# Optimization experiments

Hardware: AMD Instinct MI355X
Metric: run time of the kernel (lower is better)

## Reference

```python
import jax, jax.numpy as jnp
import numpy as np

VOC, OUT, HID, CUR = 50257, 512, 64, 16
B, S = 32, 4096
EPS = 1e-5


def _ln(x, g, b):
    m = jnp.mean(x, axis=-1, keepdims=True)
    v = jnp.mean((x - m) ** 2, axis=-1, keepdims=True)
    return (x - m) * jax.lax.rsqrt(v + EPS) * g + b


def setup_inputs() -> dict:
    key = jax.random.key(0)
    ks = jax.random.split(key, 12)
    sd = 0.02
    return {
        "x": jax.random.randint(ks[0], (B, S), 0, VOC, dtype=jnp.int64),
        "emb": jax.random.normal(ks[1], (VOC, CUR), jnp.float32) * sd,
        "Wq": jax.random.normal(ks[2], (CUR, CUR), jnp.float32) * sd,
        "bq": jnp.zeros((CUR,), jnp.float32),
        "Wk": jax.random.normal(ks[3], (CUR, CUR), jnp.float32) * sd,
        "bk": jnp.zeros((CUR,), jnp.float32),
        "Wv": jax.random.normal(ks[4], (CUR, CUR), jnp.float32) * sd,
        "bv": jnp.zeros((CUR,), jnp.float32),
        "g_lim": jnp.ones((CUR,), jnp.float32),
        "b_lim": jnp.zeros((CUR,), jnp.float32),
        "Ws": jax.random.normal(ks[5], (HID + CUR, HID), jnp.float32) * sd,
        "bs": jnp.zeros((HID,), jnp.float32),
        "g_doubt": jnp.ones((HID,), jnp.float32),
        "b_doubt": jnp.zeros((HID,), jnp.float32),
        "Wd": jax.random.normal(ks[6], (HID + CUR, OUT), jnp.float32) * sd,
        "bd": jnp.zeros((OUT,), jnp.float32),
        "g_check": jnp.ones((OUT,), jnp.float32),
        "b_check": jnp.zeros((OUT,), jnp.float32),
    }


def reference(x, emb, Wq, bq, Wk, bk, Wv, bv, g_lim, b_lim, Ws, bs,
              g_doubt, b_doubt, Wd, bd, g_check, b_check):
    Bsz, Slen = x.shape
    n_chunks = Slen // CUR
    # [n_chunks, B, CUR] token ids per chunk
    xc = x.reshape(Bsz, n_chunks, CUR).transpose(1, 0, 2)
    sus0 = jnp.zeros((Bsz, CUR, HID), emb.dtype)
    scale = 1.0 / np.sqrt(CUR)

    def step(sus, ids):
        read = emb[ids]                                  # [B, CUR, CUR]
        q = read @ Wq + bq
        k = read @ Wk + bk
        v = read @ Wv + bv
        scores = jnp.einsum('bqd,bkd->bqk', q, k) * scale
        watch = jnp.einsum('bqk,bkd->bqd', jax.nn.softmax(scores, axis=-1), v)
        watch = _ln(watch, g_lim, b_lim)                 # dropout = identity (eval)
        combined = jnp.concatenate([watch, sus], axis=-1)  # [B, CUR, HID+CUR]
        sus_new = _ln(jax.nn.gelu(combined @ Ws + bs, approximate=False),
                      g_doubt, b_doubt)
        out = _ln(combined @ Wd + bd, g_check, b_check)  # [B, CUR, OUT]
        return sus_new, out

    _, outs = jax.lax.scan(step, sus0, xc)               # [n_chunks, B, CUR, OUT]
    return outs.transpose(1, 0, 2, 3).reshape(Bsz, Slen, OUT)
```

## Files before the change

kernel.cpp:

```cpp
#include <hip/hip_runtime.h>
#include <math.h>

#define VOCN 50257
#define OUTD 512
#define HIDD 64
#define CURD 16
#define BB   32
#define SS   4096
#define NCH  256
#define KDIM 80
#define LNEPS 1e-5f

#define WS_WHI   41943040
#define WS_WLO   (WS_WHI + 96*512*2)
#define WS_FLAGS (WS_WLO + 96*512*2)
#define NRECB    128
#define NOUTB    512
#define NTASKS   4096
#define NSLABS   16

#define DPP_ADD(x, ctrl) \
    ((x) + __int_as_float(__builtin_amdgcn_update_dpp( \
        0, __float_as_int(x), (ctrl), 0xf, 0xf, true)))

__device__ __forceinline__ float row16_sum(float x) {
    x = DPP_ADD(x, 0xB1);
    x = DPP_ADD(x, 0x4E);
    x = DPP_ADD(x, 0x141);
    x = DPP_ADD(x, 0x140);
    return x;
}

__device__ __forceinline__ float wave64_sum(float x) {
    float r = row16_sum(x);
    float a = __int_as_float(__builtin_amdgcn_readlane(__float_as_int(r), 0));
    float b = __int_as_float(__builtin_amdgcn_readlane(__float_as_int(r), 16));
    float c = __int_as_float(__builtin_amdgcn_readlane(__float_as_int(r), 32));
    float d = __int_as_float(__builtin_amdgcn_readlane(__float_as_int(r), 48));
    return (a + b) + (c + d);
}

__device__ __forceinline__ unsigned short f2bf(float x) {
    unsigned u = __float_as_uint(x);
    u += 0x7fffu + ((u >> 16) & 1u);
    return (unsigned short)(u >> 16);
}
__device__ __forceinline__ float bf2f(unsigned short h) {
    return __uint_as_float(((unsigned)h) << 16);
}

typedef __attribute__((ext_vector_type(8))) short bf16x8;
typedef __attribute__((ext_vector_type(4))) float f32x4;

__global__ __launch_bounds__(256) void attn_kernel(
    const int* __restrict__ x, const float* __restrict__ emb,
    const float* __restrict__ Wq, const float* __restrict__ bq,
    const float* __restrict__ Wk, const float* __restrict__ bk,
    const float* __restrict__ Wv, const float* __restrict__ bv,
    const float* __restrict__ g_lim, const float* __restrict__ b_lim,
    float* __restrict__ combined,
    const float* __restrict__ Wd,
    unsigned short* __restrict__ whi, unsigned short* __restrict__ wlo,
    unsigned int* __restrict__ flags)
{
    if (blockIdx.x == 0) {
        flags[threadIdx.x] = 0u;
        flags[threadIdx.x + 256] = 0u;
    }

    const int wid  = threadIdx.x >> 6;
    const int lane = threadIdx.x & 63;
    const int tile = blockIdx.x * 4 + wid;
    const int t = tile >> 5, b = tile & 31;
    const int i  = lane >> 2;
    const int jg = lane & 3;
    const int j0 = jg * 4;

    __shared__ __align__(16) float ldsT[4][4][16][20];
    float (*R)[20] = ldsT[wid][0];
    float (*Q)[20] = ldsT[wid][1];
    float (*K)[20] = ldsT[wid][2];
    float (*V)[20] = ldsT[wid][3];

    int myid = 0;
    if (lane < 16) myid = x[b * SS + t * CURD + lane];
    const int id_i = __shfl(myid, i, 64);

    float4 r4 = *(const float4*)(emb + (size_t)id_i * CURD + j0);
    *(float4*)&R[i][j0] = r4;

    float rrow[16];
    {
        float4 t0 = *(const float4*)&R[i][0];
        float4 t1 = *(const float4*)&R[i][4];
        float4 t2 = *(const float4*)&R[i][8];
        float4 t3 = *(const float4*)&R[i][12];
        rrow[0]=t0.x; rrow[1]=t0.y; rrow[2]=t0.z;  rrow[3]=t0.w;
        rrow[4]=t1.x; rrow[5]=t1.y; rrow[6]=t1.z;  rrow[7]=t1.w;
        rrow[8]=t2.x; rrow[9]=t2.y; rrow[10]=t2.z; rrow[11]=t2.w;
        rrow[12]=t3.x; rrow[13]=t3.y; rrow[14]=t3.z; rrow[15]=t3.w;
    }

    float4 q4 = *(const float4*)(bq + j0);
    float4 k4 = *(const float4*)(bk + j0);
    float4 v4 = *(const float4*)(bv + j0);
    #pragma unroll
    for (int k = 0; k < 16; ++k) {
        float rv = rrow[k];
        float4 wq4 = *(const float4*)(Wq + k * CURD + j0);
        float4 wk4 = *(const float4*)(Wk + k * CURD + j0);
        float4 wv4 = *(const float4*)(Wv + k * CURD + j0);
        q4.x = fmaf(rv, wq4.x, q4.x); q4.y = fmaf(rv, wq4.y, q4.y);
        q4.z = fmaf(rv, wq4.z, q4.z); q4.w = fmaf(rv, wq4.w, q4.w);
        k4.x = fmaf(rv, wk4.x, k4.x); k4.y = fmaf(rv, wk4.y, k4.y);
        k4.z = fmaf(rv, wk4.z, k4.z); k4.w = fmaf(rv, wk4.w, k4.w);
        v4.x = fmaf(rv, wv4.x, v4.x); v4.y = fmaf(rv, wv4.y, v4.y);
        v4.z = fmaf(rv, wv4.z, v4.z); v4.w = fmaf(rv, wv4.w, v4.w);
    }
    *(float4*)&Q[i][j0] = q4;
    *(float4*)&K[i][j0] = k4;
    *(float4*)&V[i][j0] = v4;

    float qrow[16];
    {
        float4 t0 = *(const float4*)&Q[i][0];
        float4 t1 = *(const float4*)&Q[i][4];
        float4 t2 = *(const float4*)&Q[i][8];
        float4 t3 = *(const float4*)&Q[i][12];
        qrow[0]=t0.x; qrow[1]=t0.y; qrow[2]=t0.z;  qrow[3]=t0.w;
        qrow[4]=t1.x; qrow[5]=t1.y; qrow[6]=t1.z;  qrow[7]=t1.w;
        qrow[8]=t2.x; qrow[9]=t2.y; qrow[10]=t2.z; qrow[11]=t2.w;
        qrow[12]=t3.x; qrow[13]=t3.y; qrow[14]=t3.z; qrow[15]=t3.w;
    }
    float sc[4];
    #pragma unroll
    for (int jj = 0; jj < 4; ++jj) {
        const int row = j0 + jj;
        float4 c0 = *(const float4*)&K[row][0];
        float4 c1 = *(const float4*)&K[row][4];
        float4 c2 = *(const float4*)&K[row][8];
        float4 c3 = *(const float4*)&K[row][12];
        float d0 = qrow[0]*c0.x + qrow[1]*c0.y + qrow[2]*c0.z + qrow[3]*c0.w;
        float d1 = qrow[4]*c1.x + qrow[5]*c1.y + qrow[6]*c1.z + qrow[7]*c1.w;
        float d2 = qrow[8]*c2.x + qrow[9]*c2.y + qrow[10]*c2.z + qrow[11]*c2.w;
        float d3 = qrow[12]*c3.x + qrow[13]*c3.y + qrow[14]*c3.z + qrow[15]*c3.w;
        sc[jj] = ((d0 + d1) + (d2 + d3)) * 0.25f;
    }

    float mx = fmaxf(fmaxf(sc[0], sc[1]), fmaxf(sc[2], sc[3]));
    mx = fmaxf(mx, __shfl_xor(mx, 1));
    mx = fmaxf(mx, __shfl_xor(mx, 2));
    float e0 = expf(sc[0]-mx), e1 = expf(sc[1]-mx),
          e2 = expf(sc[2]-mx), e3 = expf(sc[3]-mx);
    float es = (e0 + e1) + (e2 + e3);
    es += __shfl_xor(es, 1);
    es += __shfl_xor(es, 2);
    float rs = 1.f / es;
    float4 p4 = make_float4(e0*rs, e1*rs, e2*rs, e3*rs);
    *(float4*)&R[i][j0] = p4;

    float prow[16];
    {
        float4 t0 = *(const float4*)&R[i][0];
        float4 t1 = *(const float4*)&R[i][4];
        float4 t2 = *(const float4*)&R[i][8];
        float4 t3 = *(const float4*)&R[i][12];
        prow[0]=t0.x; prow[1]=t0.y; prow[2]=t0.z;  prow[3]=t0.w;
        prow[4]=t1.x; prow[5]=t1.y; prow[6]=t1.z;  prow[7]=t1.w;
        prow[8]=t2.x; prow[9]=t2.y; prow[10]=t2.z; prow[11]=t2.w;
        prow[12]=t3.x; prow[13]=t3.y; prow[14]=t3.z; prow[15]=t3.w;
    }
    float4 w4 = make_float4(0.f, 0.f, 0.f, 0.f);
    #pragma unroll
    for (int k = 0; k < 16; ++k) {
        float4 vk = *(const float4*)&V[k][j0];
        float pv = prow[k];
        w4.x = fmaf(pv, vk.x, w4.x); w4.y = fmaf(pv, vk.y, w4.y);
        w4.z = fmaf(pv, vk.z, w4.z); w4.w = fmaf(pv, vk.w, w4.w);
    }

    float s1 = (w4.x + w4.y) + (w4.z + w4.w);
    float s2 = (w4.x*w4.x + w4.y*w4.y) + (w4.z*w4.z + w4.w*w4.w);
    s1 += __shfl_xor(s1, 1); s1 += __shfl_xor(s1, 2);
    s2 += __shfl_xor(s2, 1); s2 += __shfl_xor(s2, 2);
    float m   = s1 * (1.f / 16.f);
    float var = s2 * (1.f / 16.f) - m * m;
    float inv = rsqrtf(var + LNEPS);
    float4 gl = *(const float4*)(g_lim + j0);
    float4 bl = *(const float4*)(b_lim + j0);
    float4 o;
    o.x = (w4.x - m) * inv * gl.x + bl.x;
    o.y = (w4.y - m) * inv * gl.y + bl.y;
    o.z = (w4.z - m) * inv * gl.z + bl.z;
    o.w = (w4.w - m) * inv * gl.w + bl.w;
    *(float4*)(combined + ((size_t)tile * CURD + i) * KDIM + j0) = o;

    if (blockIdx.x < 192) {
        int idx = blockIdx.x * 256 + threadIdx.x;
        int k = idx / 512, c = idx % 512;
        float v = (k < KDIM) ? Wd[(size_t)k * OUTD + c] : 0.f;
        unsigned short h = f2bf(v);
        unsigned short l = f2bf(v - bf2f(h));
        int s = k >> 5, kk = k & 31, g = kk >> 3, e = kk & 7;
        size_t o2 = (((size_t)(s * 512 + c)) * 4 + g) * 8 + e;
        whi[o2] = h;
        wlo[o2] = l;
    }
}

__global__ __launch_bounds__(256, 1) void fused_kernel(
    const float* __restrict__ Ws, const float* __restrict__ bs,
    const float* __restrict__ g_doubt, const float* __restrict__ b_doubt,
    float* __restrict__ combined,
    const unsigned short* __restrict__ Bhi,
    const unsigned short* __restrict__ Blo,
    const float* __restrict__ bd, const float* __restrict__ g_check,
    const float* __restrict__ b_check, float* __restrict__ out,
    unsigned int* __restrict__ flags)
{
    __shared__ __align__(16) unsigned short Ahi[32][104];
    __shared__ __align__(16) unsigned short Alo[32][104];
    __shared__ float red[4][32][2];
    __shared__ float s_G[4][64];
    __shared__ int s_tk;

    const int tid = threadIdx.x;
    if (tid == 0)
        s_tk = (int)__hip_atomic_fetch_add(&flags[0], 1u,
                    __ATOMIC_RELAXED, __HIP_MEMORY_SCOPE_AGENT);
    __syncthreads();
    const int role_tk = s_tk;

    if (role_tk < NRECB) {
        __builtin_amdgcn_s_setprio(1);
        const int wid = tid >> 6;
        const int c   = tid & 63;
        const int chain = role_tk * 4 + wid;
        const int b = chain >> 4;
        const int r = chain & 15;

        float Wsw[16];
        #pragma unroll
        for (int j = 0; j < 16; ++j) Wsw[j] = Ws[j * HIDD + c];

        float Wsp[64];
        float u = 0.f, w0 = 0.f;
        #pragma unroll
        for (int j = 0; j < 64; ++j) {
            float w   = Ws[(16 + j) * HIDD + c];
            float gdj = g_doubt[j];
            float bdj = b_doubt[j];
            Wsp[j] = gdj * w;
            u += Wsp[j];
            w0 = fmaf(bdj, w, w0);
        }
        const float bsc  = bs[c];
        const float gd_c = g_doubt[c];
        const float bd_c = b_doubt[c];

        size_t rowoff = ((size_t)b * CURD + r) * KDIM;
        const size_t stride = (size_t)BB * CURD * KDIM;

        float4 wc0, wc1, wc2, wc3;
        float4 wn0, wn1, wn2, wn3;
        {
            const float4* p0 = (const float4*)(combined + rowoff);
            wc0 = p0[0]; wc1 = p0[1]; wc2 = p0[2]; wc3 = p0[3];
            const float4* p1 = (const float4*)(combined + rowoff + stride);
            wn0 = p1[0]; wn1 = p1[1]; wn2 = p1[2]; wn3 = p1[3];
        }

        float P = 0.f, mp = 0.f, ip = 0.f, w0f = 0.f;
        float sv_store = 0.f;

        for (int t = 0; t < NCH; ++t) {
            __hip_atomic_store(&combined[rowoff + 16 + c], sv_store,
                               __ATOMIC_RELAXED, __HIP_MEMORY_SCOPE_AGENT);

            if ((t & 15) == 15) {
                asm volatile("s_waitcnt vmcnt(0)" ::: "memory");
                if (c == 0)
                    __hip_atomic_fetch_add(&flags[16 + (t >> 4) * 16], 1u,
                        __ATOMIC_RELAXED, __HIP_MEMORY_SCOPE_AGENT);
            }

            float4 wp0, wp1, wp2, wp3;
            if (t + 2 < NCH) {
                const float4* p2 = (const float4*)(combined + rowoff + 2 * stride);
                wp0 = p2[0]; wp1 = p2[1]; wp2 = p2[2]; wp3 = p2[3];
            } else {
                wp0 = wp1 = wp2 = wp3 = make_float4(0.f, 0.f, 0.f, 0.f);
            }

            float h0 = fmaf(ip, P - mp * u, bsc + w0f);
            float h1 = 0.f, h2 = 0.f, h3 = 0.f;
            h0 = fmaf(wc0.x, Wsw[0],  h0); h1 = fmaf(wc0.y, Wsw[1],  h1);
            h2 = fmaf(wc0.z, Wsw[2],  h2); h3 = fmaf(wc0.w, Wsw[3],  h3);
            h0 = fmaf(wc1.x, Wsw[4],  h0); h1 = fmaf(wc1.y, Wsw[5],  h1);
            h2 = fmaf(wc1.z, Wsw[6],  h2); h3 = fmaf(wc1.w, Wsw[7],  h3);
            h0 = fmaf(wc2.x, Wsw[8],  h0); h1 = fmaf(wc2.y, Wsw[9],  h1);
            h2 = fmaf(wc2.z, Wsw[10], h2); h3 = fmaf(wc2.w, Wsw[11], h3);
            h0 = fmaf(wc3.x, Wsw[12], h0); h1 = fmaf(wc3.y, Wsw[13], h1);
            h2 = fmaf(wc3.z, Wsw[14], h2); h3 = fmaf(wc3.w, Wsw[15], h3);
            float h = (h0 + h1) + (h2 + h3);

            float G = 0.5f * h * (1.f + erff(h * 0.70710678118654752f));

            s_G[wid][c] = G;
            const float4* gp = (const float4*)s_G[wid];

            float s1 = wave64_sum(G);
            float s2 = wave64_sum(G * G);
            float m   = s1 * (1.f / 64.f);
            float var = s2 * (1.f / 64.f) - m * m;
            float inv = rsqrtf(var + LNEPS);

            float p0=0.f,p1=0.f,p2=0.f,p3=0.f,p4=0.f,p5=0.f,p6=0.f,p7=0.f;
            #pragma unroll
            for (int bq = 0; bq < 4; ++bq) {
                float4 x0 = gp[bq*4+0], x1 = gp[bq*4+1];
                float4 x2 = gp[bq*4+2], x3 = gp[bq*4+3];
                p0 = fmaf(x0.x, Wsp[16*bq+0],  p0);
                p1 = fmaf(x0.y, Wsp[16*bq+1],  p1);
                p2 = fmaf(x0.z, Wsp[16*bq+2],  p2);
                p3 = fmaf(x0.w, Wsp[16*bq+3],  p3);
                p4 = fmaf(x1.x, Wsp[16*bq+4],  p4);
                p5 = fmaf(x1.y, Wsp[16*bq+5],  p5);
                p6 = fmaf(x1.z, Wsp[16*bq+6],  p6);
                p7 = fmaf(x1.w, Wsp[16*bq+7],  p7);
                p0 = fmaf(x2.x, Wsp[16*bq+8],  p0);
                p1 = fmaf(x2.y, Wsp[16*bq+9],  p1);
                p2 = fmaf(x2.z, Wsp[16*bq+10], p2);
                p3 = fmaf(x2.w, Wsp[16*bq+11], p3);
                p4 = fmaf(x3.x, Wsp[16*bq+12], p4);
                p5 = fmaf(x3.y, Wsp[16*bq+13], p5);
                p6 = fmaf(x3.z, Wsp[16*bq+14], p6);
                p7 = fmaf(x3.w, Wsp[16*bq+15], p7);
            }
            P = ((p0 + p1) + (p2 + p3)) + ((p4 + p5) + (p6 + p7));

            sv_store = fmaf((G - m) * inv, gd_c, bd_c);
            mp = m; ip = inv; w0f = w0;
            wc0 = wn0; wc1 = wn1; wc2 = wn2; wc3 = wn3;
            wn0 = wp0; wn1 = wp1; wn2 = wp2; wn3 = wp3;
            rowoff += stride;
        }
        return;
    }

    const int lane  = tid & 63;
    const int wid   = tid >> 6;
    const int arowb = lane & 15;
    const int kg    = lane >> 4;

    int cols[8]; float bdv[8], gcv[8], bcv[8];
    #pragma unroll
    for (int n = 0; n < 8; ++n) {
        cols[n] = wid * 128 + n * 16 + arowb;
        bdv[n] = bd[cols[n]];
        gcv[n] = g_check[cols[n]];
        bcv[n] = b_check[cols[n]];
    }

    for (;;) {
        if (tid == 0)
            s_tk = (int)__hip_atomic_fetch_add(&flags[1], 1u,
                        __ATOMIC_RELAXED, __HIP_MEMORY_SCOPE_AGENT);
        __syncthreads();
        const int task = s_tk;
        if (task >= NTASKS) break;

        const int slab = task >> 8;
        if (tid == 0) {
            unsigned guard = 0;
            while (__hip_atomic_load(&flags[16 + slab * 16], __ATOMIC_RELAXED,
                                     __HIP_MEMORY_SCOPE_AGENT) < 512u
                   && guard < (1u << 20)) {
                __builtin_amdgcn_s_sleep(32);
                ++guard;
            }
        }
        __syncthreads();
        asm volatile("" ::: "memory");

        const size_t rowbase = (size_t)task * 32;

        {
            const float4* src4 = (const float4*)(combined + rowbase * KDIM);
            #pragma unroll
            for (int u2 = 0; u2 < 3; ++u2) {
                int idx = tid + 256 * u2;
                if (idx < 32 * 20) {
                    float4 v = src4[idx];
                    int rr = idx / 20, k4 = idx % 20;
                    float vs[4] = {v.x, v.y, v.z, v.w};
                    #pragma unroll
                    for (int e = 0; e < 4; ++e) {
                        unsigned short h = f2bf(vs[e]);
                        Ahi[rr][k4 * 4 + e] = h;
                        Alo[rr][k4 * 4 + e] = f2bf(vs[e] - bf2f(h));
                    }
                }
            }
            #pragma unroll
            for (int u2 = 0; u2 < 2; ++u2) {
                int idx = tid + 256 * u2;
                int rr = idx >> 4, kk = 80 + (idx & 15);
                Ahi[rr][kk] = 0;
                Alo[rr][kk] = 0;
            }
        }
        __syncthreads();

        bf16x8 a_hi[2][3], a_lo[2][3];
        #pragma unroll
        for (int ms = 0; ms < 2; ++ms)
            #pragma unroll
            for (int s = 0; s < 3; ++s) {
                a_hi[ms][s] = *(const bf16x8*)&Ahi[ms * 16 + arowb][s * 32 + kg * 8];
                a_lo[ms][s] = *(const bf16x8*)&Alo[ms * 16 + arowb][s * 32 + kg * 8];
            }

        f32x4 acc[2][8];
        #pragma unroll
        for (int ms = 0; ms < 2; ++ms)
            #pragma unroll
            for (int n = 0; n < 8; ++n) acc[ms][n] = (f32x4){0.f, 0.f, 0.f, 0.f};

        #pragma unroll
        for (int n = 0; n < 8; ++n) {
            #pragma unroll
            for (int s = 0; s < 3; ++s) {
                size_t off = (((size_t)(s * 512 + cols[n])) * 4 + kg) * 8;
                bf16x8 bh = *(const bf16x8*)(Bhi + off);
                bf16x8 bl = *(const bf16x8*)(Blo + off);
                acc[0][n] = __builtin_amdgcn_mfma_f32_16x16x32_bf16(a_hi[0][s], bh, acc[0][n], 0, 0, 0);
                acc[1][n] = __builtin_amdgcn_mfma_f32_16x16x32_bf16(a_hi[1][s], bh, acc[1][n], 0, 0, 0);
                acc[0][n] = __builtin_amdgcn_mfma_f32_16x16x32_bf16(a_lo[0][s], bh, acc[0][n], 0, 0, 0);
                acc[1][n] = __builtin_amdgcn_mfma_f32_16x16x32_bf16(a_lo[1][s], bh, acc[1][n], 0, 0, 0);
                acc[0][n] = __builtin_amdgcn_mfma_f32_16x16x32_bf16(a_hi[0][s], bl, acc[0][n], 0, 0, 0);
                acc[1][n] = __builtin_amdgcn_mfma_f32_16x16x32_bf16(a_hi[1][s], bl, acc[1][n], 0, 0, 0);
            }
        }

        #pragma unroll
        for (int ms = 0; ms < 2; ++ms) {
            float s1[4] = {0.f, 0.f, 0.f, 0.f};
            float s2[4] = {0.f, 0.f, 0.f, 0.f};
            #pragma unroll
            for (int n = 0; n < 8; ++n) {
                #pragma unroll
                for (int j = 0; j < 4; ++j) {
                    float v = acc[ms][n][j] + bdv[n];
                    acc[ms][n][j] = v;
                    s1[j] += v;
                    s2[j] = fmaf(v, v, s2[j]);
                }
            }
            #pragma unroll
            for (int j = 0; j < 4; ++j) {
                s1[j] = row16_sum(s1[j]);
                s2[j] = row16_sum(s2[j]);
            }
            if (arowb == 0) {
                #pragma unroll
                for (int j = 0; j < 4; ++j) {
                    red[wid][ms * 16 + kg * 4 + j][0] = s1[j];
                    red[wid][ms * 16 + kg * 4 + j][1] = s2[j];
                }
            }
        }
        __syncthreads();

        #pragma unroll
        for (int ms = 0; ms < 2; ++ms) {
            #pragma unroll
            for (int j = 0; j < 4; ++j) {
                const int rowl = ms * 16 + kg * 4 + j;
                float t1 = (red[0][rowl][0] + red[1][rowl][0])
                         + (red[2][rowl][0] + red[3][rowl][0]);
                float t2 = (red[0][rowl][1] + red[1][rowl][1])
                         + (red[2][rowl][1] + red[3][rowl][1]);
                float mm  = t1 * (1.f / 512.f);
                float var = t2 * (1.f / 512.f) - mm * mm;
                float iv  = rsqrtf(var + LNEPS);

                size_t R = rowbase + (size_t)rowl;
                int ii  = (int)(R & 15);
                int bb2 = (int)((R >> 4) & 31);
                int tt  = (int)(R >> 9);
                size_t orow = ((size_t)bb2 * SS + (size_t)tt * CURD + ii) * OUTD;

                #pragma unroll
                for (int n = 0; n < 8; ++n) {
                    out[orow + cols[n]] =
                        (acc[ms][n][j] - mm) * iv * gcv[n] + bcv[n];
                }
            }
        }
        __syncthreads();
    }
}

extern "C" void kernel_launch(void* const* d_in, const int* in_sizes, int n_in,
                              void* d_out, int out_size, void* d_ws, size_t ws_size,
                              hipStream_t stream)
{
    const int*   x       = (const int*)  d_in[0];
    const float* emb     = (const float*)d_in[1];
    const float* Wq      = (const float*)d_in[2];
    const float* bq      = (const float*)d_in[3];
    const float* Wk      = (const float*)d_in[4];
    const float* bk      = (const float*)d_in[5];
    const float* Wv      = (const float*)d_in[6];
    const float* bv      = (const float*)d_in[7];
    const float* g_lim   = (const float*)d_in[8];
    const float* b_lim   = (const float*)d_in[9];
    const float* Ws      = (const float*)d_in[10];
    const float* bs      = (const float*)d_in[11];
    const float* g_doubt = (const float*)d_in[12];
    const float* b_doubt = (const float*)d_in[13];
    const float* Wd      = (const float*)d_in[14];
    const float* bd      = (const float*)d_in[15];
    const float* g_check = (const float*)d_in[16];
    const float* b_check = (const float*)d_in[17];

    float* out      = (float*)d_out;
    float* combined = (float*)d_ws;
    unsigned short* whi = (unsigned short*)((char*)d_ws + WS_WHI);
    unsigned short* wlo = (unsigned short*)((char*)d_ws + WS_WLO);
    unsigned int*  flags = (unsigned int*)((char*)d_ws + WS_FLAGS);

    attn_kernel<<<dim3(NCH * BB / 4), dim3(256), 0, stream>>>(
        x, emb, Wq, bq, Wk, bk, Wv, bv, g_lim, b_lim, combined,
        Wd, whi, wlo, flags);

    fused_kernel<<<dim3(NRECB + NOUTB), dim3(256), 0, stream>>>(
        Ws, bs, g_doubt, b_doubt, combined, whi, wlo,
        bd, g_check, b_check, out, flags);
}
```

Baseline: 579.3 us.

## Preload each recurrence chain's watch rows into LDS and halve waves per block

```diff
diff --git a/kernel.cpp b/kernel.cpp
--- a/kernel.cpp
+++ b/kernel.cpp
@@ -14,7 +14,7 @@
 #define WS_WHI   41943040
 #define WS_WLO   (WS_WHI + 96*512*2)
 #define WS_FLAGS (WS_WLO + 96*512*2)
-#define NRECB    128
+#define NRECB    256
 #define NOUTB    512
 #define NTASKS   4096
 #define NSLABS   16
@@ -208,6 +208,18 @@
     }
 }
 
+union LdsU {
+    struct {
+        float watch[2][NCH][16];
+        float G[2][64];
+    } rec;
+    struct {
+        unsigned short Ahi[32][104];
+        unsigned short Alo[32][104];
+        float red[4][32][2];
+    } o;
+};
+
 __global__ __launch_bounds__(256, 1) void fused_kernel(
     const float* __restrict__ Ws, const float* __restrict__ bs,
     const float* __restrict__ g_doubt, const float* __restrict__ b_doubt,
@@ -218,10 +230,7 @@
     const float* __restrict__ b_check, float* __restrict__ out,
     unsigned int* __restrict__ flags)
 {
-    __shared__ __align__(16) unsigned short Ahi[32][104];
-    __shared__ __align__(16) unsigned short Alo[32][104];
-    __shared__ float red[4][32][2];
-    __shared__ float s_G[4][64];
+    __shared__ __align__(16) LdsU lds;
     __shared__ int s_tk;
 
     const int tid = threadIdx.x;
@@ -232,12 +241,26 @@
     const int role_tk = s_tk;
 
     if (role_tk < NRECB) {
+        const int wid = tid >> 6;
+        if (wid >= 2) return;
         __builtin_amdgcn_s_setprio(1);
-        const int wid = tid >> 6;
         const int c   = tid & 63;
-        const int chain = role_tk * 4 + wid;
+        const int lane = c;
+        const int chain = role_tk * 2 + wid;
         const int b = chain >> 4;
         const int r = chain & 15;
+
+        {
+            const int tt4 = lane >> 2;
+            const int j4  = lane & 3;
+            #pragma unroll
+            for (int p = 0; p < 16; ++p) {
+                int t = p * 16 + tt4;
+                float4 v = *(const float4*)(combined
+                    + ((size_t)(t * BB + b) * CURD + r) * KDIM + j4 * 4);
+                *(float4*)&lds.rec.watch[wid][t][j4 * 4] = v;
+            }
+        }
 
         float Wsw[16];
         #pragma unroll
@@ -261,14 +284,8 @@
         size_t rowoff = ((size_t)b * CURD + r) * KDIM;
         const size_t stride = (size_t)BB * CURD * KDIM;
 
-        float4 wc0, wc1, wc2, wc3;
-        float4 wn0, wn1, wn2, wn3;
-        {
-            const float4* p0 = (const float4*)(combined + rowoff);
-            wc0 = p0[0]; wc1 = p0[1]; wc2 = p0[2]; wc3 = p0[3];
-            const float4* p1 = (const float4*)(combined + rowoff + stride);
-            wn0 = p1[0]; wn1 = p1[1]; wn2 = p1[2]; wn3 = p1[3];
-        }
+        const float4* wrow0 = (const float4*)&lds.rec.watch[wid][0][0];
+        float4 wc0 = wrow0[0], wc1 = wrow0[1], wc2 = wrow0[2], wc3 = wrow0[3];
 
         float P = 0.f, mp = 0.f, ip = 0.f, w0f = 0.f;
         float sv_store = 0.f;
@@ -282,14 +299,6 @@
                 if (c == 0)
                     __hip_atomic_fetch_add(&flags[16 + (t >> 4) * 16], 1u,
                         __ATOMIC_RELAXED, __HIP_MEMORY_SCOPE_AGENT);
-            }
-
-            float4 wp0, wp1, wp2, wp3;
-            if (t + 2 < NCH) {
-                const float4* p2 = (const float4*)(combined + rowoff + 2 * stride);
-                wp0 = p2[0]; wp1 = p2[1]; wp2 = p2[2]; wp3 = p2[3];
-            } else {
-                wp0 = wp1 = wp2 = wp3 = make_float4(0.f, 0.f, 0.f, 0.f);
             }
 
             float h0 = fmaf(ip, P - mp * u, bsc + w0f);
@@ -306,8 +315,12 @@
 
             float G = 0.5f * h * (1.f + erff(h * 0.70710678118654752f));
 
-            s_G[wid][c] = G;
-            const float4* gp = (const float4*)s_G[wid];
+            lds.rec.G[wid][c] = G;
+            const float4* gp = (const float4*)lds.rec.G[wid];
+
+            const int tn = (t + 1 < NCH) ? t + 1 : t;
+            const float4* wrow = (const float4*)&lds.rec.watch[wid][tn][0];
+            float4 wn0 = wrow[0], wn1 = wrow[1], wn2 = wrow[2], wn3 = wrow[3];
 
             float s1 = wave64_sum(G);
             float s2 = wave64_sum(G * G);
@@ -342,7 +355,6 @@
             sv_store = fmaf((G - m) * inv, gd_c, bd_c);
             mp = m; ip = inv; w0f = w0;
             wc0 = wn0; wc1 = wn1; wc2 = wn2; wc3 = wn3;
-            wn0 = wp0; wn1 = wp1; wn2 = wp2; wn3 = wp3;
             rowoff += stride;
         }
         return;
@@ -397,8 +409,8 @@
                     #pragma unroll
                     for (int e = 0; e < 4; ++e) {
                         unsigned short h = f2bf(vs[e]);
-                        Ahi[rr][k4 * 4 + e] = h;
-                        Alo[rr][k4 * 4 + e] = f2bf(vs[e] - bf2f(h));
+                        lds.o.Ahi[rr][k4 * 4 + e] = h;
+                        lds.o.Alo[rr][k4 * 4 + e] = f2bf(vs[e] - bf2f(h));
                     }
                 }
             }
@@ -406,8 +418,8 @@
             for (int u2 = 0; u2 < 2; ++u2) {
                 int idx = tid + 256 * u2;
                 int rr = idx >> 4, kk = 80 + (idx & 15);
-                Ahi[rr][kk] = 0;
-                Alo[rr][kk] = 0;
+                lds.o.Ahi[rr][kk] = 0;
+                lds.o.Alo[rr][kk] = 0;
             }
         }
         __syncthreads();
@@ -417,8 +429,8 @@
         for (int ms = 0; ms < 2; ++ms)
             #pragma unroll
             for (int s = 0; s < 3; ++s) {
-                a_hi[ms][s] = *(const bf16x8*)&Ahi[ms * 16 + arowb][s * 32 + kg * 8];
-                a_lo[ms][s] = *(const bf16x8*)&Alo[ms * 16 + arowb][s * 32 + kg * 8];
+                a_hi[ms][s] = *(const bf16x8*)&lds.o.Ahi[ms * 16 + arowb][s * 32 + kg * 8];
+                a_lo[ms][s] = *(const bf16x8*)&lds.o.Alo[ms * 16 + arowb][s * 32 + kg * 8];
             }
 
         f32x4 acc[2][8];
@@ -465,8 +477,8 @@
             if (arowb == 0) {
                 #pragma unroll
                 for (int j = 0; j < 4; ++j) {
-                    red[wid][ms * 16 + kg * 4 + j][0] = s1[j];
-                    red[wid][ms * 16 + kg * 4 + j][1] = s2[j];
+                    lds.o.red[wid][ms * 16 + kg * 4 + j][0] = s1[j];
+                    lds.o.red[wid][ms * 16 + kg * 4 + j][1] = s2[j];
                 }
             }
         }
@@ -477,10 +489,10 @@
             #pragma unroll
             for (int j = 0; j < 4; ++j) {
                 const int rowl = ms * 16 + kg * 4 + j;
-                float t1 = (red[0][rowl][0] + red[1][rowl][0])
-                         + (red[2][rowl][0] + red[3][rowl][0]);
-                float t2 = (red[0][rowl][1] + red[1][rowl][1])
-                         + (red[2][rowl][1] + red[3][rowl][1]);
+                float t1 = (lds.o.red[0][rowl][0] + lds.o.red[1][rowl][0])
+                         + (lds.o.red[2][rowl][0] + lds.o.red[3][rowl][0]);
+                float t2 = (lds.o.red[0][rowl][1] + lds.o.red[1][rowl][1])
+                         + (lds.o.red[2][rowl][1] + lds.o.red[3][rowl][1]);
                 float mm  = t1 * (1.f / 512.f);
                 float var = t2 * (1.f / 512.f) - mm * mm;
                 float iv  = rsqrtf(var + LNEPS);
```

Result: faster. 552.8 us (-4.6%).
